# Kernel optimization log

Hardware: AMD Instinct MI355X
Metric: run time of the kernel (lower is better)

The kernel has to match this reference:

```python
import jax, jax.numpy as jnp
import numpy as np

N_NODES = 20000
N_EDGES = 320000
N_FEAT = 128
MLP_HID = 64
N_GRAPHS = 16
N_LAYERS = 5
EPS = 1e-5


def setup_inputs() -> dict:
    key = jax.random.key(0)
    ks = jax.random.split(key, 8)
    x = jax.random.normal(ks[0], (N_NODES, N_FEAT), dtype=jnp.float32)
    edge_index = jax.random.randint(ks[1], (2, N_EDGES), 0, N_NODES, dtype=jnp.int64)
    batch = jnp.sort(jax.random.randint(ks[2], (N_NODES,), 0, N_GRAPHS, dtype=jnp.int64))
    W1 = jax.random.normal(ks[3], (N_LAYERS, N_FEAT, MLP_HID), dtype=jnp.float32) * 0.05
    b1 = jnp.zeros((N_LAYERS, MLP_HID), dtype=jnp.float32)
    W2 = jax.random.normal(ks[4], (N_LAYERS, MLP_HID, N_FEAT), dtype=jnp.float32) * 0.05
    b2 = jnp.zeros((N_LAYERS, N_FEAT), dtype=jnp.float32)
    gn_weight = jnp.ones((N_LAYERS, N_FEAT), dtype=jnp.float32)
    gn_bias = jnp.zeros((N_LAYERS, N_FEAT), dtype=jnp.float32)
    gn_scale = jnp.ones((N_LAYERS, N_FEAT), dtype=jnp.float32)
    lin_w = jax.random.normal(ks[5], (N_FEAT, 1), dtype=jnp.float32) * 0.05
    lin_b = jnp.zeros((1,), dtype=jnp.float32)
    return {"x": x, "edge_index": edge_index, "batch": batch,
            "W1": W1, "b1": b1, "W2": W2, "b2": b2,
            "gn_weight": gn_weight, "gn_bias": gn_bias, "gn_scale": gn_scale,
            "lin_w": lin_w, "lin_b": lin_b}


def _conv(h, src, dst, W1, b1, W2, b2):
    # message MLP is per-source-node, so compute MLP(x) once per node,
    # then gather by src and scatter-add to dst. Self loops add m[i] at i.
    m = jax.nn.relu(h @ W1 + b1) @ W2 + b2  # [N, C]
    return jax.ops.segment_sum(m[src], dst, num_segments=N_NODES) + m


def _graph_norm(h, batch, cnt, w, b, a):
    mean = jax.ops.segment_sum(h, batch, num_segments=N_GRAPHS) / cnt  # [G, C]
    out = h - a * mean[batch]
    var = jax.ops.segment_sum(out * out, batch, num_segments=N_GRAPHS) / cnt
    out = out * jax.lax.rsqrt(var[batch] + EPS)
    return w * out + b


def reference(x, edge_index, batch, W1, b1, W2, b2, gn_weight, gn_bias, gn_scale, lin_w, lin_b):
    src, dst = edge_index[0], edge_index[1]
    cnt = jax.ops.segment_sum(jnp.ones((N_NODES, 1), x.dtype), batch,
                              num_segments=N_GRAPHS)
    cnt = jnp.maximum(cnt, 1.0)  # [G, 1]
    h = x
    for i in range(N_LAYERS):
        g = _conv(h, src, dst, W1[i], b1[i], W2[i], b2[i])
        g = _graph_norm(g, batch, cnt, gn_weight[i], gn_bias[i], gn_scale[i])
        g = jax.nn.relu(g)  # dropout is identity in eval mode
        h = g if i == 0 else g + h  # residual from layer 2 onward
    pooled = jax.ops.segment_sum(h, batch, num_segments=N_GRAPHS) / cnt  # [G, C]
    return pooled @ lin_w + lin_b  # [G, 1]
```

## Files before the change

### kernel.cpp

```cpp
#include <hip/hip_runtime.h>

#define N_NODES 20000
#define N_EDGES 320000
#define N_FEAT 128
#define MLP_HID 64
#define N_GRAPHS 16
#define N_LAYERS 5
#define EPS 1e-5f

typedef __attribute__((ext_vector_type(8))) short short8;
typedef __attribute__((ext_vector_type(4))) float f32x4;

__device__ inline float bf2f(unsigned short u) { return __uint_as_float(((unsigned)u) << 16); }
__device__ inline unsigned short f2bf(float f) {
  unsigned u = __float_as_uint(f);
  u += 0x7FFF + ((u >> 16) & 1);
  return (unsigned short)(u >> 16);
}


__global__ __launch_bounds__(256) void k_prep(const float* __restrict__ W1, const float* __restrict__ W2,
                                              unsigned short* __restrict__ w1t, unsigned short* __restrict__ w2t,
                                              int* __restrict__ deg, float* __restrict__ zero_region) {
  int idx = blockIdx.x * 256 + threadIdx.x;
  if (idx < 20000) deg[idx] = 0;
  if (idx < 22528) zero_region[idx] = 0.0f;
  if (idx < 40960) {
    int l = idx >> 13, rem = idx & 8191;
    int n = rem >> 7, k = rem & 127;
    w1t[idx] = f2bf(W1[l * 8192 + k * 64 + n]);
  } else {
    int j = idx - 40960;
    int l = j >> 13, rem = j & 8191;
    int n = rem >> 6, k = rem & 63;
    w2t[j] = f2bf(W2[l * 8192 + k * 128 + n]);
  }
}


__global__ __launch_bounds__(256) void k_deg(const int* __restrict__ dst, int* __restrict__ deg) {
  int e = blockIdx.x * 256 + threadIdx.x;
  atomicAdd(&deg[dst[e]], 1);
}

__global__ __launch_bounds__(1024) void k_scan(const int* __restrict__ deg, int* __restrict__ rowptr,
                                               int* __restrict__ cursor, const int* __restrict__ batch,
                                               float* __restrict__ cntf) {
  __shared__ int sdata[1024];
  __shared__ int spos[17];
  constexpr int CH = 20;
  int t = threadIdx.x;
  int base = t * CH;
  int loc[CH];
  int partial = 0;
#pragma unroll
  for (int i = 0; i < CH; i++) {
    int idx = base + i;
    int v = (idx < N_NODES) ? deg[idx] : 0;
    loc[i] = v;
    partial += v;
  }
  sdata[t] = partial;
  __syncthreads();
  for (int off = 1; off < 1024; off <<= 1) {
    int v = (t >= off) ? sdata[t - off] : 0;
    __syncthreads();
    sdata[t] += v;
    __syncthreads();
  }
  int run = sdata[t] - partial;
#pragma unroll
  for (int i = 0; i < CH; i++) {
    int idx = base + i;
    if (idx < N_NODES) {
      rowptr[idx] = run;
      cursor[idx] = run;
      run += loc[i];
    }
  }
  if (t == 1023) rowptr[N_NODES] = sdata[1023];
  if (t < 17) {
    int lo = 0, hi = N_NODES;
    while (lo < hi) {
      int mid = (lo + hi) >> 1;
      if (batch[mid] < t) lo = mid + 1; else hi = mid;
    }
    spos[t] = lo;
  }
  __syncthreads();
  if (t < N_GRAPHS) cntf[t] = fmaxf((float)(spos[t + 1] - spos[t]), 1.0f);
}

__global__ __launch_bounds__(256) void k_fill(const int* __restrict__ src, const int* __restrict__ dst,
                                              int* __restrict__ cursor, int* __restrict__ src_sorted) {
  int e = blockIdx.x * 256 + threadIdx.x;
  int d = dst[e];
  int p = atomicAdd(&cursor[d], 1);
  src_sorted[p] = src[e];
}


#define PADK 136
#define PADH 72

__global__ __launch_bounds__(256) void k_mlp(const float* __restrict__ hin, unsigned short* __restrict__ mout,
                                             const unsigned short* __restrict__ w1t,
                                             const unsigned short* __restrict__ w2t,
                                             const float* __restrict__ b1, const float* __restrict__ b2) {
  __shared__ __align__(16) short hS[64 * PADK];
  __shared__ __align__(16) short w1S[64 * PADK];
  __shared__ __align__(16) short hidS[64 * PADH];
  __shared__ __align__(16) short w2S[128 * PADH];
  __shared__ float b1S[64];
  __shared__ float b2S[128];
  int t = threadIdx.x;
  int r0 = blockIdx.x * 64;
#pragma unroll
  for (int i = 0; i < 8; i++) {
    int idx = t + i * 256;
    int row = idx >> 5, c4 = idx & 31;
    float4 v = (r0 + row < N_NODES) ? ((const float4*)hin)[(size_t)(r0 + row) * 32 + c4]
                                    : make_float4(0.f, 0.f, 0.f, 0.f);
    ushort4 s;
    s.x = f2bf(v.x); s.y = f2bf(v.y); s.z = f2bf(v.z); s.w = f2bf(v.w);
    *(ushort4*)&hS[row * PADK + c4 * 4] = s;
  }
#pragma unroll
  for (int i = 0; i < 4; i++) {
    int idx = t + i * 256;
    *(int4*)&w1S[(idx >> 4) * PADK + (idx & 15) * 8] = ((const int4*)w1t)[idx];
    *(int4*)&w2S[(idx >> 3) * PADH + (idx & 7) * 8] = ((const int4*)w2t)[idx];
  }
  if (t < 64) b1S[t] = b1[t];
  else if (t < 192) b2S[t - 64] = b2[t - 64];
  __syncthreads();

  int w = t >> 6, lane = t & 63, lm = lane & 15, quad = lane >> 4;
  int mrow = w * 16 + lm;
  int orow = w * 16 + quad * 4;

  f32x4 zero = {0.f, 0.f, 0.f, 0.f};
  f32x4 acc[4] = {zero, zero, zero, zero};
#pragma unroll
  for (int k0 = 0; k0 < 128; k0 += 32) {
    short8 a = *(const short8*)&hS[mrow * PADK + k0 + quad * 8];
#pragma unroll
    for (int nt = 0; nt < 4; nt++) {
      short8 b = *(const short8*)&w1S[(nt * 16 + lm) * PADK + k0 + quad * 8];
      acc[nt] = __builtin_amdgcn_mfma_f32_16x16x32_bf16(a, b, acc[nt], 0, 0, 0);
    }
  }
#pragma unroll
  for (int nt = 0; nt < 4; nt++) {
    int col = nt * 16 + lm;
    float bb = b1S[col];
#pragma unroll
    for (int r = 0; r < 4; r++)
      hidS[(orow + r) * PADH + col] = (short)f2bf(fmaxf(acc[nt][r] + bb, 0.0f));
  }
  __syncthreads();

  f32x4 acc2[8] = {zero, zero, zero, zero, zero, zero, zero, zero};
#pragma unroll
  for (int k0 = 0; k0 < 64; k0 += 32) {
    short8 a = *(const short8*)&hidS[mrow * PADH + k0 + quad * 8];
#pragma unroll
    for (int nt = 0; nt < 8; nt++) {
      short8 b = *(const short8*)&w2S[(nt * 16 + lm) * PADH + k0 + quad * 8];
      acc2[nt] = __builtin_amdgcn_mfma_f32_16x16x32_bf16(a, b, acc2[nt], 0, 0, 0);
    }
  }
#pragma unroll
  for (int nt = 0; nt < 8; nt++) {
    int col = nt * 16 + lm;
    float bb = b2S[col];
#pragma unroll
    for (int r = 0; r < 4; r++)
      hS[(orow + r) * PADK + col] = (short)f2bf(acc2[nt][r] + bb);
  }
  __syncthreads();
#pragma unroll
  for (int i = 0; i < 4; i++) {
    int idx = t + i * 256;
    int row = idx >> 4, cc = idx & 15;
    if (r0 + row < N_NODES)
      ((int4*)mout)[(size_t)(r0 + row) * 16 + cc] = *(const int4*)&hS[row * PADK + cc * 8];
  }
}


__global__ __launch_bounds__(256) void k_scatterS(const unsigned short* __restrict__ mbf, float* __restrict__ g,
                                                  const int* __restrict__ rowptr, const int* __restrict__ srcs,
                                                  const int* __restrict__ batch,
                                                  float* __restrict__ s1, float* __restrict__ s2) {
  __shared__ float gR[4 * 128];
  int t = threadIdx.x;
  int w = t >> 6;
  int node = blockIdx.x * 4 + w;
  int lane = t & 63;
  int quarter = lane >> 4;
  int q16 = lane & 15;
  const float4* m4 = (const float4*)mbf;
  float acc[8];
  union BU { float4 f; unsigned short u[8]; };
  if (quarter == 0) {
    BU U; U.f = m4[(size_t)node * 16 + q16];
#pragma unroll
    for (int j = 0; j < 8; j++) acc[j] = bf2f(U.u[j]);
  } else {
#pragma unroll
    for (int j = 0; j < 8; j++) acc[j] = 0.0f;
  }
  int e = rowptr[node], e1 = rowptr[node + 1];
  for (; e + 16 <= e1; e += 16) {
    int i0 = srcs[e + quarter];
    int i1 = srcs[e + 4 + quarter];
    int i2 = srcs[e + 8 + quarter];
    int i3 = srcs[e + 12 + quarter];
    BU U0, U1, U2, U3;
    U0.f = m4[(size_t)i0 * 16 + q16];
    U1.f = m4[(size_t)i1 * 16 + q16];
    U2.f = m4[(size_t)i2 * 16 + q16];
    U3.f = m4[(size_t)i3 * 16 + q16];
#pragma unroll
    for (int j = 0; j < 8; j++)
      acc[j] += (bf2f(U0.u[j]) + bf2f(U1.u[j])) + (bf2f(U2.u[j]) + bf2f(U3.u[j]));
  }
  for (; e + 4 <= e1; e += 4) {
    BU U0; U0.f = m4[(size_t)srcs[e + quarter] * 16 + q16];
#pragma unroll
    for (int j = 0; j < 8; j++) acc[j] += bf2f(U0.u[j]);
  }
  if (e + quarter < e1) {
    BU U0; U0.f = m4[(size_t)srcs[e + quarter] * 16 + q16];
#pragma unroll
    for (int j = 0; j < 8; j++) acc[j] += bf2f(U0.u[j]);
  }
#pragma unroll
  for (int j = 0; j < 8; j++) {
    acc[j] += __shfl_xor(acc[j], 16);
    acc[j] += __shfl_xor(acc[j], 32);
  }
  if (quarter == 0) {
    float4 lo = make_float4(acc[0], acc[1], acc[2], acc[3]);
    float4 hi = make_float4(acc[4], acc[5], acc[6], acc[7]);
    float4* g4 = (float4*)(g + (size_t)node * 128 + q16 * 8);
    g4[0] = lo;
    g4[1] = hi;
    *(float4*)&gR[w * 128 + q16 * 8] = lo;
    *(float4*)&gR[w * 128 + q16 * 8 + 4] = hi;
  }
  __syncthreads();
  int n0 = blockIdx.x * 4;
  if (batch[n0] == batch[n0 + 3]) {
    int gg = batch[n0];
    if (t < 128) {
      float s = gR[t] + gR[128 + t] + gR[256 + t] + gR[384 + t];
      atomicAdd(&s1[gg * 128 + t], s);
    } else {
      int c = t - 128;
      float v0 = gR[c], v1 = gR[128 + c], v2 = gR[256 + c], v3 = gR[384 + c];
      atomicAdd(&s2[gg * 128 + c], v0 * v0 + v1 * v1 + v2 * v2 + v3 * v3);
    }
  } else {
    if (t < 128) {
#pragma unroll
      for (int r = 0; r < 4; r++) atomicAdd(&s1[batch[n0 + r] * 128 + t], gR[r * 128 + t]);
    } else {
      int c = t - 128;
#pragma unroll
      for (int r = 0; r < 4; r++) {
        float v = gR[r * 128 + c];
        atomicAdd(&s2[batch[n0 + r] * 128 + c], v * v);
      }
    }
  }
}


__global__ __launch_bounds__(256) void k_apply(const float* __restrict__ gin, float* __restrict__ h,
                                               const int* __restrict__ batch,
                                               const float* __restrict__ s1, const float* __restrict__ s2,
                                               const float* __restrict__ cntf,
                                               const float* __restrict__ w, const float* __restrict__ b,
                                               const float* __restrict__ a, int residual) {
  int idx = blockIdx.x * 256 + threadIdx.x;
  int n = idx >> 5, c4 = idx & 31;
  int gg = batch[n];
  float invc = 1.0f / cntf[gg];
  float4 sm = ((const float4*)s1)[gg * 32 + c4];
  float4 se = ((const float4*)s2)[gg * 32 + c4];
  float4 av = ((const float4*)a)[c4];
  float4 wv = ((const float4*)w)[c4];
  float4 bv = ((const float4*)b)[c4];
  float4 gv = ((const float4*)gin)[idx];
  float4 hv = make_float4(0.f, 0.f, 0.f, 0.f);
  if (residual) hv = ((const float4*)h)[idx];
  float4 o;
#define APPLY1(X)                                                          \
  {                                                                        \
    float mean = sm.X * invc;                                              \
    float ex2 = se.X * invc;                                               \
    float ac = av.X;                                                       \
    float var = fmaxf(ex2 - mean * mean * (2.0f * ac - ac * ac), 0.0f);    \
    float d = gv.X - ac * mean;                                            \
    float y = wv.X * (d * rsqrtf(var + EPS)) + bv.X;                       \
    y = fmaxf(y, 0.0f);                                                    \
    o.X = residual ? (y + hv.X) : y;                                       \
  }
  APPLY1(x) APPLY1(y) APPLY1(z) APPLY1(w)
#undef APPLY1
  ((float4*)h)[idx] = o;
}


__global__ __launch_bounds__(256) void k_applyPool(const float* __restrict__ gin, const float* __restrict__ h,
                                                   const int* __restrict__ batch,
                                                   const float* __restrict__ s1, const float* __restrict__ s2,
                                                   const float* __restrict__ cntf,
                                                   const float* __restrict__ gw, const float* __restrict__ gb,
                                                   const float* __restrict__ ga, float* __restrict__ pooled) {
  __shared__ float4 poolT[256];
  int t = threadIdx.x;
  int idx = blockIdx.x * 256 + t;
  int n = idx >> 5, c4 = idx & 31;
  int gg = batch[n];
  float invc = 1.0f / cntf[gg];
  float4 sm = ((const float4*)s1)[gg * 32 + c4];
  float4 se = ((const float4*)s2)[gg * 32 + c4];
  float4 av = ((const float4*)ga)[c4];
  float4 wv = ((const float4*)gw)[c4];
  float4 bv = ((const float4*)gb)[c4];
  float4 gv = ((const float4*)gin)[idx];
  float4 hv = ((const float4*)h)[idx];
  float4 o;
#define APPLY1(X)                                                          \
  {                                                                        \
    float mean = sm.X * invc;                                              \
    float ex2 = se.X * invc;                                               \
    float ac = av.X;                                                       \
    float var = fmaxf(ex2 - mean * mean * (2.0f * ac - ac * ac), 0.0f);    \
    float d = gv.X - ac * mean;                                            \
    float y = wv.X * (d * rsqrtf(var + EPS)) + bv.X;                       \
    o.X = fmaxf(y, 0.0f) + hv.X;                                           \
  }
  APPLY1(x) APPLY1(y) APPLY1(z) APPLY1(w)
#undef APPLY1
  poolT[t] = o;
  __syncthreads();
  int n0 = blockIdx.x * 8;
  if (batch[n0] == batch[n0 + 7]) {
    if (t < 32) {
      float4 s = poolT[t];
#pragma unroll
      for (int r = 1; r < 8; r++) {
        float4 v = poolT[r * 32 + t];
        s.x += v.x; s.y += v.y; s.z += v.z; s.w += v.w;
      }
      int gt = batch[n0];
      atomicAdd(&pooled[gt * 128 + t * 4 + 0], s.x);
      atomicAdd(&pooled[gt * 128 + t * 4 + 1], s.y);
      atomicAdd(&pooled[gt * 128 + t * 4 + 2], s.z);
      atomicAdd(&pooled[gt * 128 + t * 4 + 3], s.w);
    }
  } else {
    atomicAdd(&pooled[gg * 128 + c4 * 4 + 0], o.x);
    atomicAdd(&pooled[gg * 128 + c4 * 4 + 1], o.y);
    atomicAdd(&pooled[gg * 128 + c4 * 4 + 2], o.z);
    atomicAdd(&pooled[gg * 128 + c4 * 4 + 3], o.w);
  }
}


__global__ __launch_bounds__(256) void k_final(const float* __restrict__ pooled, const float* __restrict__ cntf,
                                               const float* __restrict__ lw, const float* __restrict__ lb,
                                               float* __restrict__ out) {
  int lane = threadIdx.x & 63, wave = threadIdx.x >> 6;
  for (int gi = 0; gi < 4; gi++) {
    int gidx = wave * 4 + gi;
    float s = pooled[gidx * 128 + lane] * lw[lane] + pooled[gidx * 128 + 64 + lane] * lw[64 + lane];
    for (int o = 32; o >= 1; o >>= 1) s += __shfl_down(s, o);
    if (lane == 0) out[gidx] = s / cntf[gidx] + lb[0];
  }
}


extern "C" void kernel_launch(void* const* d_in, const int* in_sizes, int n_in,
                              void* d_out, int out_size, void* d_ws, size_t ws_size,
                              hipStream_t stream) {
  const float* x = (const float*)d_in[0];
  const int* ei = (const int*)d_in[1];
  const int* batch = (const int*)d_in[2];
  const float* W1 = (const float*)d_in[3];
  const float* b1 = (const float*)d_in[4];
  const float* W2 = (const float*)d_in[5];
  const float* b2 = (const float*)d_in[6];
  const float* gnw = (const float*)d_in[7];
  const float* gnb = (const float*)d_in[8];
  const float* gna = (const float*)d_in[9];
  const float* lw = (const float*)d_in[10];
  const float* lb = (const float*)d_in[11];
  float* out = (float*)d_out;

  const int* srcI = ei;
  const int* dstI = ei + N_EDGES;

  char* p = (char*)d_ws;
  float* hbuf = (float*)(p + 0);
  unsigned short* mbuf = (unsigned short*)(p + 10240000);
  float* gbuf = (float*)(p + 15360000);
  int* src_sorted = (int*)(p + 25600000);
  int* rowptr = (int*)(p + 26880000);
  int* cursor = (int*)(p + 26960128);
  int* deg = (int*)(p + 27040256);
  float* cntf = (float*)(p + 27120384);
  unsigned short* w1t = (unsigned short*)(p + 27120512);
  unsigned short* w2t = (unsigned short*)(p + 27202432);
  float* sbufs = (float*)(p + 27284352);
  float* pooled = (float*)(p + 27366272);

  k_prep<<<320, 256, 0, stream>>>(W1, W2, w1t, w2t, deg, sbufs);
  k_deg<<<N_EDGES / 256, 256, 0, stream>>>(dstI, deg);
  k_scan<<<1, 1024, 0, stream>>>(deg, rowptr, cursor, batch, cntf);
  k_fill<<<N_EDGES / 256, 256, 0, stream>>>(srcI, dstI, cursor, src_sorted);

  const float* hin = x;
  for (int i = 0; i < N_LAYERS; i++) {
    float* s1 = sbufs + (size_t)i * 4096;
    float* s2 = s1 + 2048;
    k_mlp<<<(N_NODES + 63) / 64, 256, 0, stream>>>(hin, mbuf, w1t + (size_t)i * 8192, w2t + (size_t)i * 8192,
                                                   b1 + (size_t)i * 64, b2 + (size_t)i * 128);
    k_scatterS<<<N_NODES / 4, 256, 0, stream>>>(mbuf, gbuf, rowptr, src_sorted, batch, s1, s2);
    if (i < N_LAYERS - 1) {
      k_apply<<<N_NODES * N_FEAT / 4 / 256, 256, 0, stream>>>(gbuf, hbuf, batch, s1, s2, cntf,
                                                              gnw + (size_t)i * 128, gnb + (size_t)i * 128,
                                                              gna + (size_t)i * 128, i > 0 ? 1 : 0);
      hin = hbuf;
    }
  }

  k_applyPool<<<N_NODES * N_FEAT / 4 / 256, 256, 0, stream>>>(
      gbuf, hbuf, batch, sbufs + 4 * 4096, sbufs + 4 * 4096 + 2048, cntf,
      gnw + 4 * 128, gnb + 4 * 128, gna + 4 * 128, pooled);
  k_final<<<1, 256, 0, stream>>>(pooled, cntf, lw, lb, out);
}
```

Measured before the change: 407.8 us.

## Split graph-norm statistics out of the scatter kernel into a separate stats kernel

Removes the shared-memory staging, block-wide barrier and per-block atomics for the GraphNorm sum and sum-of-squares from the gather/scatter kernel. A new kernel re-reads the aggregated features, accumulates per-graph sums over 8-node chunks, and flushes with atomics only when the graph id changes. This unfuses work, adding one extra launch and an extra 10 MB read of the aggregated buffer per layer. In exchange the scatter kernel gets lighter and the atomic count drops.

```diff
diff --git a/kernel.cpp b/kernel.cpp
--- a/kernel.cpp
+++ b/kernel.cpp
@@ -189,15 +189,10 @@
 }
 
 
-__global__ __launch_bounds__(256) void k_scatterS(const unsigned short* __restrict__ mbf, float* __restrict__ g,
-                                                  const int* __restrict__ rowptr, const int* __restrict__ srcs,
-                                                  const int* __restrict__ batch,
-                                                  float* __restrict__ s1, float* __restrict__ s2) {
-  __shared__ float gR[4 * 128];
-  int t = threadIdx.x;
-  int w = t >> 6;
-  int node = blockIdx.x * 4 + w;
-  int lane = t & 63;
+__global__ __launch_bounds__(256) void k_scatter(const unsigned short* __restrict__ mbf, float* __restrict__ g,
+                                                 const int* __restrict__ rowptr, const int* __restrict__ srcs) {
+  int node = (blockIdx.x * 256 + threadIdx.x) >> 6;
+  int lane = threadIdx.x & 63;
   int quarter = lane >> 4;
   int q16 = lane & 15;
   const float4* m4 = (const float4*)mbf;
@@ -242,39 +237,37 @@
     acc[j] += __shfl_xor(acc[j], 32);
   }
   if (quarter == 0) {
-    float4 lo = make_float4(acc[0], acc[1], acc[2], acc[3]);
-    float4 hi = make_float4(acc[4], acc[5], acc[6], acc[7]);
     float4* g4 = (float4*)(g + (size_t)node * 128 + q16 * 8);
-    g4[0] = lo;
-    g4[1] = hi;
-    *(float4*)&gR[w * 128 + q16 * 8] = lo;
-    *(float4*)&gR[w * 128 + q16 * 8 + 4] = hi;
-  }
-  __syncthreads();
-  int n0 = blockIdx.x * 4;
-  if (batch[n0] == batch[n0 + 3]) {
-    int gg = batch[n0];
-    if (t < 128) {
-      float s = gR[t] + gR[128 + t] + gR[256 + t] + gR[384 + t];
-      atomicAdd(&s1[gg * 128 + t], s);
-    } else {
-      int c = t - 128;
-      float v0 = gR[c], v1 = gR[128 + c], v2 = gR[256 + c], v3 = gR[384 + c];
-      atomicAdd(&s2[gg * 128 + c], v0 * v0 + v1 * v1 + v2 * v2 + v3 * v3);
-    }
-  } else {
-    if (t < 128) {
-#pragma unroll
-      for (int r = 0; r < 4; r++) atomicAdd(&s1[batch[n0 + r] * 128 + t], gR[r * 128 + t]);
-    } else {
-      int c = t - 128;
-#pragma unroll
-      for (int r = 0; r < 4; r++) {
-        float v = gR[r * 128 + c];
-        atomicAdd(&s2[batch[n0 + r] * 128 + c], v * v);
-      }
-    }
-  }
+    g4[0] = make_float4(acc[0], acc[1], acc[2], acc[3]);
+    g4[1] = make_float4(acc[4], acc[5], acc[6], acc[7]);
+  }
+}
+
+
+#define STAT_CHUNK 8
+
+__global__ __launch_bounds__(128) void k_stats(const float* __restrict__ in, const int* __restrict__ batch,
+                                               float* __restrict__ s1, float* __restrict__ s2) {
+  int n0 = blockIdx.x * STAT_CHUNK;
+  int c = threadIdx.x;
+  int curg = batch[n0];
+  float a1 = 0.0f, a2 = 0.0f;
+#pragma unroll
+  for (int k = 0; k < STAT_CHUNK; k++) {
+    int n = n0 + k;
+    int gg = batch[n];
+    if (gg != curg) {
+      atomicAdd(&s1[curg * 128 + c], a1);
+      atomicAdd(&s2[curg * 128 + c], a2);
+      a1 = 0.0f; a2 = 0.0f;
+      curg = gg;
+    }
+    float v = in[(size_t)n * 128 + c];
+    a1 += v;
+    a2 += v * v;
+  }
+  atomicAdd(&s1[curg * 128 + c], a1);
+  atomicAdd(&s2[curg * 128 + c], a2);
 }
 
 
@@ -430,7 +423,8 @@
     float* s2 = s1 + 2048;
     k_mlp<<<(N_NODES + 63) / 64, 256, 0, stream>>>(hin, mbuf, w1t + (size_t)i * 8192, w2t + (size_t)i * 8192,
                                                    b1 + (size_t)i * 64, b2 + (size_t)i * 128);
-    k_scatterS<<<N_NODES / 4, 256, 0, stream>>>(mbuf, gbuf, rowptr, src_sorted, batch, s1, s2);
+    k_scatter<<<N_NODES / 4, 256, 0, stream>>>(mbuf, gbuf, rowptr, src_sorted);
+    k_stats<<<N_NODES / STAT_CHUNK, 128, 0, stream>>>(gbuf, batch, s1, s2);
     if (i < N_LAYERS - 1) {
       k_apply<<<N_NODES * N_FEAT / 4 / 256, 256, 0, stream>>>(gbuf, hbuf, batch, s1, s2, cntf,
                                                               gnw + (size_t)i * 128, gnb + (size_t)i * 128,
```

Result: faster. 351.5 us (-13.8%).
